# Kernel tuning notes

Measured on AMD Instinct MI355X. Metric: run time of the kernel, lower is better.

The kernel has to match this reference:

```python
import jax, jax.numpy as jnp
import numpy as np

B = 256
NUM_CAPS = 2            # digit capsules
N_IN = 6 * 6 * 6 * 32   # 6912 input capsules
D_OUT = 16
D_IN = 8
N_ROUTING = 3           # original loops range(3 - 1) = 2 iterations
EPS = 1e-9


def squash(s):
    # squash along last axis: (|s|^2/(1+|s|^2)) * s/|s|
    n2 = jnp.sum(s * s, axis=-1, keepdims=True)
    return (n2 / (1.0 + n2)) * s / jnp.sqrt(n2 + EPS)


def setup_inputs() -> dict:
    key = jax.random.key(0)
    k1, k2 = jax.random.split(key)
    x = jax.random.normal(k1, (B, N_IN, D_IN), dtype=jnp.float32)
    W = jax.random.normal(k2, (NUM_CAPS, N_IN, D_OUT, D_IN), dtype=jnp.float32) * 0.1
    return {"x": x, "W": W}


def reference(x, W):
    # tile x over the 2 digit capsules + per-(capsule, input-capsule) matvec:
    # u_hat[b,j,n,e] = sum_d W[j,n,e,d] * x[b,n,d]   -> [B, 2, N, 16]
    u_hat = jnp.einsum('bnd,jned->bjne', x, W)
    b_logits = jnp.zeros(u_hat.shape[:3], dtype=x.dtype)  # [B, 2, N]
    v = None
    for _ in range(N_ROUTING - 1):
        c = jax.nn.softmax(b_logits, axis=1)               # softmax over the 2 capsules (dim=1 in source)
        s = jnp.einsum('bjn,bjne->bje', c, u_hat)          # [B, 2, 16]
        v = squash(s)
        b_logits = b_logits + jnp.einsum('bje,bjne->bjn', v, u_hat)
    return v
```

## Files before the change

kernel.cpp:

```cpp
#include <hip/hip_runtime.h>

#define B_ 256
#define J_ 2
#define N_ 6912
#define E_ 16
#define D_ 8
#define NBT 12
#define CGX 576
#define TOT4 (J_*NBT*32)
#define XROW 25
#define XTOT4 (64*XROW)

__device__ __forceinline__ float dpp_add8(float v){
  v += __int_as_float(__builtin_amdgcn_update_dpp(0, __float_as_int(v), 0xB1,  0xF, 0xF, true));
  v += __int_as_float(__builtin_amdgcn_update_dpp(0, __float_as_int(v), 0x4E,  0xF, 0xF, true));
  v += __int_as_float(__builtin_amdgcn_update_dpp(0, __float_as_int(v), 0x141, 0xF, 0xF, true));
  return v;
}

__device__ __forceinline__ float dot8(const float4 wa, const float4 wb,
                                      const float4 xa, const float4 xb, float a){
  a = fmaf(wa.x, xa.x, a); a = fmaf(wa.y, xa.y, a);
  a = fmaf(wa.z, xa.z, a); a = fmaf(wa.w, xa.w, a);
  a = fmaf(wb.x, xb.x, a); a = fmaf(wb.y, xb.y, a);
  a = fmaf(wb.z, xb.z, a); a = fmaf(wb.w, xb.w, a);
  return a;
}

__device__ __forceinline__ void stageWX(const float* __restrict__ W,
                                        const float* __restrict__ x,
                                        int nb0, int by64, int tid,
                                        float4* __restrict__ Wl,
                                        float4* __restrict__ Xl){
  float4 bw[3], bx[6];
  #pragma unroll
  for (int r=0;r<3;++r){
    const int idx = r*256 + tid;
    const int j  = (idx >= NBT*32) ? 1 : 0;
    const int r4 = idx - j*(NBT*32);
    bw[r] = *(const float4*)(W + ((size_t)j*N_ + nb0)*(E_*D_) + (size_t)r4*4);
  }
  #pragma unroll
  for (int r=0;r<6;++r){
    const int g = r*256 + tid;
    const int brow = g/24, c = g - brow*24;
    bx[r] = *(const float4*)(x + ((size_t)(by64 + brow)*N_ + nb0)*D_ + c*4);
  }
  #pragma unroll
  for (int r=0;r<3;++r){
    const int idx = r*256 + tid;
    const int u = idx & 31;
    Wl[(idx & ~31) | (u ^ (u>>3))] = bw[r];
  }
  #pragma unroll
  for (int r=0;r<6;++r){
    const int g = r*256 + tid;
    const int brow = g/24, c = g - brow*24;
    Xl[brow*XROW + c] = bx[r];
  }
}


__global__ __launch_bounds__(256, 4) void kpass1(const float* __restrict__ x,
                                                 const float* __restrict__ W,
                                                 float* __restrict__ partial)
{
  __shared__ float4 smem4[TOT4 + XTOT4];
  float4* Wl = smem4;
  float4* Xl = smem4 + TOT4;
  const int tid  = threadIdx.x;
  const int lane = tid & 63;
  const int wv   = __builtin_amdgcn_readfirstlane(tid >> 6);
  const int eh   = lane & 7;
  const int bs   = lane >> 3;
  const int h    = wv >> 1;
  const int p    = wv & 1;
  const int nb0  = blockIdx.x * NBT;

  const int sA0 = (eh*2)       ^ ((eh*2)>>3);
  const int sB0 = (eh*2+1)     ^ ((eh*2+1)>>3);
  const int sA1 = ((eh+8)*2)   ^ (((eh+8)*2)>>3);
  const int sB1 = ((eh+8)*2+1) ^ (((eh+8)*2+1)>>3);

  stageWX(W, x, nb0, blockIdx.y*64, tid, Wl, Xl);
  __syncthreads();

  const float4* Xr = Xl + (h*32 + bs)*XROW;
  float aJ0E0[4]={0,0,0,0}, aJ0E1[4]={0,0,0,0}, aJ1E0[4]={0,0,0,0}, aJ1E1[4]={0,0,0,0};
  #pragma unroll 1
  for (int ni=p; ni<NBT; ni+=2){
    const float4 w00a = Wl[ni*32 + sA0],       w00b = Wl[ni*32 + sB0];
    const float4 w01a = Wl[ni*32 + sA1],       w01b = Wl[ni*32 + sB1];
    const float4 w10a = Wl[(NBT+ni)*32 + sA0], w10b = Wl[(NBT+ni)*32 + sB0];
    const float4 w11a = Wl[(NBT+ni)*32 + sA1], w11b = Wl[(NBT+ni)*32 + sB1];
    #pragma unroll
    for (int k=0;k<4;++k){
      const float4 xa = Xr[k*(8*XROW) + ni*2];
      const float4 xb = Xr[k*(8*XROW) + ni*2 + 1];
      aJ0E0[k] = dot8(w00a,w00b, xa,xb, aJ0E0[k]);
      aJ0E1[k] = dot8(w01a,w01b, xa,xb, aJ0E1[k]);
      aJ1E0[k] = dot8(w10a,w10b, xa,xb, aJ1E0[k]);
      aJ1E1[k] = dot8(w11a,w11b, xa,xb, aJ1E1[k]);
    }
  }

  __syncthreads();
  float* red = (float*)smem4;
  if (p == 1){
    #pragma unroll
    for (int k=0;k<4;++k){
      const int base = h*1056 + (8*k+bs)*33 + eh;
      red[base]      = aJ0E0[k];
      red[base + 8]  = aJ0E1[k];
      red[base + 16] = aJ1E0[k];
      red[base + 24] = aJ1E1[k];
    }
  }
  __syncthreads();
  if (p == 0){
    float* dst = partial + (size_t)(blockIdx.x*4 + blockIdx.y)*2048;
    #pragma unroll
    for (int k=0;k<4;++k){
      const int base = h*1056 + (8*k+bs)*33 + eh;
      const int go   = (h*32 + 8*k + bs)*32 + eh;
      dst[go]      = aJ0E0[k] + red[base];
      dst[go + 8]  = aJ0E1[k] + red[base + 8];
      dst[go + 16] = aJ1E0[k] + red[base + 16];
      dst[go + 24] = aJ1E1[k] + red[base + 24];
    }
  }
}

__global__ __launch_bounds__(256, 3) void kpass2(const float* __restrict__ x,
                                                 const float* __restrict__ W,
                                                 const float* __restrict__ v1,
                                                 float* __restrict__ partial)
{
  __shared__ float4 smem4[TOT4 + XTOT4];
  float4* Wl = smem4;
  float4* Xl = smem4 + TOT4;
  const int tid  = threadIdx.x;
  const int lane = tid & 63;
  const int wv   = __builtin_amdgcn_readfirstlane(tid >> 6);
  const int eh   = lane & 7;
  const int bs   = lane >> 3;
  const int h    = wv >> 1;
  const int p    = wv & 1;
  const int nb0  = blockIdx.x * NBT;
  const int b0g  = blockIdx.y*64;

  const int sA0 = (eh*2)       ^ ((eh*2)>>3);
  const int sB0 = (eh*2+1)     ^ ((eh*2+1)>>3);
  const int sA1 = ((eh+8)*2)   ^ (((eh+8)*2)>>3);
  const int sB1 = ((eh+8)*2+1) ^ (((eh+8)*2+1)>>3);

  stageWX(W, x, nb0, b0g, tid, Wl, Xl);
  float v00[4], v01[4], v10[4], v11[4];
  #pragma unroll
  for (int k=0;k<4;++k){
    const size_t vb = (size_t)(b0g + h*32 + 8*k + bs)*32 + eh;
    v00[k] = v1[vb];
    v01[k] = v1[vb + 8];
    v10[k] = v1[vb + 16];
    v11[k] = v1[vb + 24];
  }
  __syncthreads();

  const float4* Xr = Xl + (h*32 + bs)*XROW;
  float aJ0E0[4]={0,0,0,0}, aJ0E1[4]={0,0,0,0}, aJ1E0[4]={0,0,0,0}, aJ1E1[4]={0,0,0,0};
  #pragma unroll 1
  for (int ni=p; ni<NBT; ni+=2){
    const float4 w00a = Wl[ni*32 + sA0],       w00b = Wl[ni*32 + sB0];
    const float4 w01a = Wl[ni*32 + sA1],       w01b = Wl[ni*32 + sB1];
    const float4 w10a = Wl[(NBT+ni)*32 + sA0], w10b = Wl[(NBT+ni)*32 + sB0];
    const float4 w11a = Wl[(NBT+ni)*32 + sA1], w11b = Wl[(NBT+ni)*32 + sB1];
    #pragma unroll
    for (int k=0;k<4;++k){
      const float4 xa = Xr[k*(8*XROW) + ni*2];
      const float4 xb = Xr[k*(8*XROW) + ni*2 + 1];
      const float u00 = dot8(w00a,w00b, xa,xb, 0.f);
      const float u01 = dot8(w01a,w01b, xa,xb, 0.f);
      const float u10 = dot8(w10a,w10b, xa,xb, 0.f);
      const float u11 = dot8(w11a,w11b, xa,xb, 0.f);
      float t = v10[k]*u10;
      t = fmaf(v11[k], u11, t);
      t = fmaf(-v00[k], u00, t);
      t = fmaf(-v01[k], u01, t);
      t = dpp_add8(t);
      const float c0 = __builtin_amdgcn_rcpf(1.f + __expf(t));
      const float c1 = 1.f - c0;
      aJ0E0[k] = fmaf(c0, u00, aJ0E0[k]);
      aJ0E1[k] = fmaf(c0, u01, aJ0E1[k]);
      aJ1E0[k] = fmaf(c1, u10, aJ1E0[k]);
      aJ1E1[k] = fmaf(c1, u11, aJ1E1[k]);
    }
  }

  __syncthreads();
  float* red = (float*)smem4;
  if (p == 1){
    #pragma unroll
    for (int k=0;k<4;++k){
      const int base = h*1056 + (8*k+bs)*33 + eh;
      red[base]      = aJ0E0[k];
      red[base + 8]  = aJ0E1[k];
      red[base + 16] = aJ1E0[k];
      red[base + 24] = aJ1E1[k];
    }
  }
  __syncthreads();
  if (p == 0){
    float* dst = partial + (size_t)(blockIdx.x*4 + blockIdx.y)*2048;
    #pragma unroll
    for (int k=0;k<4;++k){
      const int base = h*1056 + (8*k+bs)*33 + eh;
      const int go   = (h*32 + 8*k + bs)*32 + eh;
      dst[go]      = aJ0E0[k] + red[base];
      dst[go + 8]  = aJ0E1[k] + red[base + 8];
      dst[go + 16] = aJ1E0[k] + red[base + 16];
      dst[go + 24] = aJ1E1[k] + red[base + 24];
    }
  }
}

template<bool HALF>
__global__ __launch_bounds__(256) void kred(const float* __restrict__ partial,
                                            float* __restrict__ dst)
{
  __shared__ float sh[128];
  const int tid  = threadIdx.x;
  const int o    = blockIdx.x*128 + (tid & 127);
  const int half = tid >> 7;
  const int btile = o >> 11, q = o & 2047;
  const float* p = partial + (size_t)btile*2048 + q + (size_t)half*(CGX/2)*8192;
  float s = 0.f;
  #pragma unroll 24
  for (int cx=0; cx<CGX/2; ++cx) s += p[(size_t)cx*8192];
  if (half) sh[tid & 127] = s;
  __syncthreads();
  if (!half){
    s += sh[tid & 127];
    if (HALF) s *= 0.5f;
    float n2 = s*s;
    #pragma unroll
    for (int m=1; m<16; m<<=1) n2 += __shfl_xor(n2, m);
    dst[o] = s * (n2/(1.f+n2)) * rsqrtf(n2 + 1e-9f);
  }
}

#define NT 512
__global__ __launch_bounds__(NT) void kmono(const float* __restrict__ x,
                                            const float* __restrict__ W,
                                            float* __restrict__ out)
{
  const int b    = blockIdx.x;
  const int tid  = threadIdx.x;
  const int wv   = tid >> 6;
  const int lane = tid & 63;
  __shared__ float wred[8*33];
  __shared__ float vsh[32];

  float acc[32];
  #pragma unroll
  for (int i=0;i<32;++i) acc[i]=0.f;
  for (int n = tid; n < N_; n += NT){
    const float4 xa = *(const float4*)(x + ((size_t)b*N_ + n)*D_);
    const float4 xb = *(const float4*)(x + ((size_t)b*N_ + n)*D_ + 4);
    #pragma unroll
    for (int j=0;j<J_;++j){
      const float* wp = W + ((size_t)j*N_ + n)*(E_*D_);
      #pragma unroll
      for (int e=0;e<E_;++e){
        const float4 wa = *(const float4*)(wp + e*8);
        const float4 wb = *(const float4*)(wp + e*8 + 4);
        float a = acc[j*16+e];
        a = fmaf(wa.x,xa.x,a); a = fmaf(wa.y,xa.y,a); a = fmaf(wa.z,xa.z,a); a = fmaf(wa.w,xa.w,a);
        a = fmaf(wb.x,xb.x,a); a = fmaf(wb.y,xb.y,a); a = fmaf(wb.z,xb.z,a); a = fmaf(wb.w,xb.w,a);
        acc[j*16+e] = a;
      }
    }
  }
  #pragma unroll
  for (int i=0;i<32;++i){
    float v = acc[i];
    #pragma unroll
    for (int off=32; off; off>>=1) v += __shfl_xor(v, off);
    acc[i] = v;
  }
  if (lane == 0){
    #pragma unroll
    for (int i=0;i<32;++i) wred[wv*33 + i] = acc[i];
  }
  __syncthreads();
  if (tid < 32){
    float s = 0.f;
    #pragma unroll
    for (int w=0;w<8;++w) s += wred[w*33 + tid];
    wred[tid] = 0.5f * s;
  }
  __syncthreads();
  if (tid < 32){
    const int j = tid >> 4; float n2 = 0.f;
    #pragma unroll
    for (int e=0;e<16;++e){ const float sv = wred[j*16+e]; n2 = fmaf(sv,sv,n2); }
    vsh[tid] = wred[tid] * (n2/(1.f+n2)) * rsqrtf(n2 + 1e-9f);
  }
  __syncthreads();
  float vv[32];
  #pragma unroll
  for (int i=0;i<32;++i) vv[i] = vsh[i];

  #pragma unroll
  for (int i=0;i<32;++i) acc[i]=0.f;
  for (int n = tid; n < N_; n += NT){
    const float4 xa = *(const float4*)(x + ((size_t)b*N_ + n)*D_);
    const float4 xb = *(const float4*)(x + ((size_t)b*N_ + n)*D_ + 4);
    float u[32];
    #pragma unroll
    for (int j=0;j<J_;++j){
      const float* wp = W + ((size_t)j*N_ + n)*(E_*D_);
      #pragma unroll
      for (int e=0;e<E_;++e){
        const float4 wa = *(const float4*)(wp + e*8);
        const float4 wb = *(const float4*)(wp + e*8 + 4);
        float a;
        a = wa.x*xa.x; a = fmaf(wa.y,xa.y,a); a = fmaf(wa.z,xa.z,a); a = fmaf(wa.w,xa.w,a);
        a = fmaf(wb.x,xb.x,a); a = fmaf(wb.y,xb.y,a); a = fmaf(wb.z,xb.z,a); a = fmaf(wb.w,xb.w,a);
        u[j*16+e] = a;
      }
    }
    float l0=0.f, l1=0.f;
    #pragma unroll
    for (int e=0;e<16;++e){ l0 = fmaf(vv[e],u[e],l0); l1 = fmaf(vv[16+e],u[16+e],l1); }
    const float c0 = 1.f/(1.f + __expf(l1 - l0));
    const float c1 = 1.f - c0;
    #pragma unroll
    for (int e=0;e<16;++e){ acc[e] = fmaf(c0,u[e],acc[e]); acc[16+e] = fmaf(c1,u[16+e],acc[16+e]); }
  }
  #pragma unroll
  for (int i=0;i<32;++i){
    float v = acc[i];
    #pragma unroll
    for (int off=32; off; off>>=1) v += __shfl_xor(v, off);
    acc[i] = v;
  }
  __syncthreads();
  if (lane == 0){
    #pragma unroll
    for (int i=0;i<32;++i) wred[wv*33 + i] = acc[i];
  }
  __syncthreads();
  if (tid < 32){
    float s = 0.f;
    #pragma unroll
    for (int w=0;w<8;++w) s += wred[w*33 + tid];
    wred[tid] = s;
  }
  __syncthreads();
  if (tid < 32){
    const int j = tid >> 4; float n2 = 0.f;
    #pragma unroll
    for (int e=0;e<16;++e){ const float sv = wred[j*16+e]; n2 = fmaf(sv,sv,n2); }
    out[(size_t)b*32 + tid] = wred[tid] * (n2/(1.f+n2)) * rsqrtf(n2 + 1e-9f);
  }
}

extern "C" void kernel_launch(void* const* d_in, const int* in_sizes, int n_in,
                              void* d_out, int out_size, void* d_ws, size_t ws_size,
                              hipStream_t stream)
{
  const float* x = (const float*)d_in[0];
  const float* W = (const float*)d_in[1];
  if (n_in >= 2 && in_sizes[0] < in_sizes[1]){
    x = (const float*)d_in[1]; W = (const float*)d_in[0];
  }
  float* out = (float*)d_out;

  const size_t need = (size_t)(8192 + (size_t)CGX*4*2048) * sizeof(float);

  if (ws_size >= need){
    float* wsf     = (float*)d_ws;
    float* v1      = wsf;
    float* partial = wsf + 8192;
    kpass1<<<dim3(CGX,4), 256, 0, stream>>>(x, W, partial);
    kred<true ><<<64, 256, 0, stream>>>(partial, v1);
    kpass2<<<dim3(CGX,4), 256, 0, stream>>>(x, W, v1, partial);
    kred<false><<<64, 256, 0, stream>>>(partial, out);
  } else {
    kmono<<<B_, NT, 0, stream>>>(x, W, out);
  }
}
```

Baseline: 144.9 us.

## Fuse reduction kernels into pass kernels via atomic completion counters

Removes the two separate reduction kernel launches by appending extra blocks to each pass kernel. These blocks spin on a global atomic counter until all producer blocks have written their partials, then perform the reduction and squash. This saves launch gaps between dependent kernels but adds a memset launch and relies on the spinning blocks not starving producers; it is safe only if the hardware dispatches lower block indices first, since the spinning blocks hold CU slots while they wait.

```diff
diff --git a/kernel.cpp b/kernel.cpp
--- a/kernel.cpp
+++ b/kernel.cpp
@@ -7,9 +7,12 @@
 #define D_ 8
 #define NBT 12
 #define CGX 576
+#define RBX 16
 #define TOT4 (J_*NBT*32)
 #define XROW 25
 #define XTOT4 (64*XROW)
+#define NPROD (CGX*4)
+#define OFS_CTR (8192 + (size_t)CGX*4*2048)
 
 __device__ __forceinline__ float dpp_add8(float v){
   v += __int_as_float(__builtin_amdgcn_update_dpp(0, __float_as_int(v), 0xB1,  0xF, 0xF, true));
@@ -60,29 +63,77 @@
   }
 }
 
+template<bool HALF>
+__device__ __forceinline__ void reduce_tail(const float* __restrict__ partial,
+                                            float* __restrict__ dst,
+                                            float* __restrict__ sh,
+                                            int r, int tid){
+  const int o    = r*128 + (tid & 127);
+  const int half = tid >> 7;
+  const int btile = o >> 11, q = o & 2047;
+  const float* p = partial + (size_t)btile*2048 + q + (size_t)half*(CGX/2)*8192;
+  float s = 0.f;
+  #pragma unroll 24
+  for (int cx=0; cx<CGX/2; ++cx) s += p[(size_t)cx*8192];
+  if (half) sh[tid & 127] = s;
+  __syncthreads();
+  if (!half){
+    s += sh[tid & 127];
+    if (HALF) s *= 0.5f;
+    float n2 = s*s;
+    #pragma unroll
+    for (int m=1; m<16; m<<=1) n2 += __shfl_xor(n2, m);
+    dst[o] = s * (n2/(1.f+n2)) * rsqrtf(n2 + 1e-9f);
+  }
+}
+
+__device__ __forceinline__ void wait_all(unsigned* ctr){
+  while (__hip_atomic_load(ctr, __ATOMIC_ACQUIRE, __HIP_MEMORY_SCOPE_AGENT) < NPROD)
+    __builtin_amdgcn_s_sleep(8);
+  __threadfence();
+}
+
+__device__ __forceinline__ void signal_done(unsigned* ctr, int tid){
+  __syncthreads();
+  if (tid == 0){
+    __threadfence();
+    __hip_atomic_fetch_add(ctr, 1u, __ATOMIC_RELEASE, __HIP_MEMORY_SCOPE_AGENT);
+  }
+}
+
 
 __global__ __launch_bounds__(256, 4) void kpass1(const float* __restrict__ x,
                                                  const float* __restrict__ W,
-                                                 float* __restrict__ partial)
+                                                 float* __restrict__ partial,
+                                                 float* __restrict__ v1,
+                                                 unsigned* __restrict__ ctr)
 {
   __shared__ float4 smem4[TOT4 + XTOT4];
+  const int tid = threadIdx.x;
+  const int bx  = blockIdx.x, by = blockIdx.y;
+
+  if (bx >= CGX){
+    wait_all(ctr);
+    reduce_tail<true>(partial, v1, (float*)smem4, (bx-CGX)*4 + by, tid);
+    return;
+  }
+
   float4* Wl = smem4;
   float4* Xl = smem4 + TOT4;
-  const int tid  = threadIdx.x;
   const int lane = tid & 63;
   const int wv   = __builtin_amdgcn_readfirstlane(tid >> 6);
   const int eh   = lane & 7;
   const int bs   = lane >> 3;
   const int h    = wv >> 1;
   const int p    = wv & 1;
-  const int nb0  = blockIdx.x * NBT;
+  const int nb0  = bx * NBT;
 
   const int sA0 = (eh*2)       ^ ((eh*2)>>3);
   const int sB0 = (eh*2+1)     ^ ((eh*2+1)>>3);
   const int sA1 = ((eh+8)*2)   ^ (((eh+8)*2)>>3);
   const int sB1 = ((eh+8)*2+1) ^ (((eh+8)*2+1)>>3);
 
-  stageWX(W, x, nb0, blockIdx.y*64, tid, Wl, Xl);
+  stageWX(W, x, nb0, by*64, tid, Wl, Xl);
   __syncthreads();
 
   const float4* Xr = Xl + (h*32 + bs)*XROW;
@@ -118,7 +169,7 @@
   }
   __syncthreads();
   if (p == 0){
-    float* dst = partial + (size_t)(blockIdx.x*4 + blockIdx.y)*2048;
+    float* dst = partial + (size_t)(bx*4 + by)*2048;
     #pragma unroll
     for (int k=0;k<4;++k){
       const int base = h*1056 + (8*k+bs)*33 + eh;
@@ -129,25 +180,36 @@
       dst[go + 24] = aJ1E1[k] + red[base + 24];
     }
   }
+  signal_done(ctr, tid);
 }
 
 __global__ __launch_bounds__(256, 3) void kpass2(const float* __restrict__ x,
                                                  const float* __restrict__ W,
                                                  const float* __restrict__ v1,
-                                                 float* __restrict__ partial)
+                                                 float* __restrict__ partial,
+                                                 float* __restrict__ out,
+                                                 unsigned* __restrict__ ctr)
 {
   __shared__ float4 smem4[TOT4 + XTOT4];
+  const int tid = threadIdx.x;
+  const int bx  = blockIdx.x, by = blockIdx.y;
+
+  if (bx >= CGX){
+    wait_all(ctr);
+    reduce_tail<false>(partial, out, (float*)smem4, (bx-CGX)*4 + by, tid);
+    return;
+  }
+
   float4* Wl = smem4;
   float4* Xl = smem4 + TOT4;
-  const int tid  = threadIdx.x;
   const int lane = tid & 63;
   const int wv   = __builtin_amdgcn_readfirstlane(tid >> 6);
   const int eh   = lane & 7;
   const int bs   = lane >> 3;
   const int h    = wv >> 1;
   const int p    = wv & 1;
-  const int nb0  = blockIdx.x * NBT;
-  const int b0g  = blockIdx.y*64;
+  const int nb0  = bx * NBT;
+  const int b0g  = by*64;
 
   const int sA0 = (eh*2)       ^ ((eh*2)>>3);
   const int sB0 = (eh*2+1)     ^ ((eh*2+1)>>3);
@@ -210,7 +272,7 @@
   }
   __syncthreads();
   if (p == 0){
-    float* dst = partial + (size_t)(blockIdx.x*4 + blockIdx.y)*2048;
+    float* dst = partial + (size_t)(bx*4 + by)*2048;
     #pragma unroll
     for (int k=0;k<4;++k){
       const int base = h*1056 + (8*k+bs)*33 + eh;
@@ -221,31 +283,7 @@
       dst[go + 24] = aJ1E1[k] + red[base + 24];
     }
   }
-}
-
-template<bool HALF>
-__global__ __launch_bounds__(256) void kred(const float* __restrict__ partial,
-                                            float* __restrict__ dst)
-{
-  __shared__ float sh[128];
-  const int tid  = threadIdx.x;
-  const int o    = blockIdx.x*128 + (tid & 127);
-  const int half = tid >> 7;
-  const int btile = o >> 11, q = o & 2047;
-  const float* p = partial + (size_t)btile*2048 + q + (size_t)half*(CGX/2)*8192;
-  float s = 0.f;
-  #pragma unroll 24
-  for (int cx=0; cx<CGX/2; ++cx) s += p[(size_t)cx*8192];
-  if (half) sh[tid & 127] = s;
-  __syncthreads();
-  if (!half){
-    s += sh[tid & 127];
-    if (HALF) s *= 0.5f;
-    float n2 = s*s;
-    #pragma unroll
-    for (int m=1; m<16; m<<=1) n2 += __shfl_xor(n2, m);
-    dst[o] = s * (n2/(1.f+n2)) * rsqrtf(n2 + 1e-9f);
-  }
+  signal_done(ctr, tid);
 }
 
 #define NT 512
@@ -376,16 +414,17 @@
   }
   float* out = (float*)d_out;
 
-  const size_t need = (size_t)(8192 + (size_t)CGX*4*2048) * sizeof(float);
+  const size_t need = (OFS_CTR + 2) * sizeof(float);
 
   if (ws_size >= need){
-    float* wsf     = (float*)d_ws;
-    float* v1      = wsf;
-    float* partial = wsf + 8192;
-    kpass1<<<dim3(CGX,4), 256, 0, stream>>>(x, W, partial);
-    kred<true ><<<64, 256, 0, stream>>>(partial, v1);
-    kpass2<<<dim3(CGX,4), 256, 0, stream>>>(x, W, v1, partial);
-    kred<false><<<64, 256, 0, stream>>>(partial, out);
+    float* wsf      = (float*)d_ws;
+    float* v1       = wsf;
+    float* partial  = wsf + 8192;
+    unsigned* ctrs  = (unsigned*)(wsf + OFS_CTR);
+
+    hipMemsetAsync(ctrs, 0, 2*sizeof(unsigned), stream);
+    kpass1<<<dim3(CGX+RBX,4), 256, 0, stream>>>(x, W, partial, v1, ctrs);
+    kpass2<<<dim3(CGX+RBX,4), 256, 0, stream>>>(x, W, v1, partial, out, ctrs+1);
   } else {
     kmono<<<B_, NT, 0, stream>>>(x, W, out);
   }
```

New measurement: 496.3 us. 243% more time.
